# Optimization experiments

Measured on AMD Instinct MI355X. Metric: run time of the kernel, lower is better.

Reference implementation:

```python
import jax, jax.numpy as jnp
import numpy as np

B, S, HID = 4, 2048, 576
NH, NKV, HD = 9, 3, 64
MAXPOS, THETA = 8192, 100000.0


def rotate_half(x):
    x1, x2 = x[..., : x.shape[-1] // 2], x[..., x.shape[-1] // 2 :]
    return jnp.concatenate((-x2, x1), axis=-1)


def setup_inputs() -> dict:
    key = jax.random.key(0)
    ks = jax.random.split(key, 6)
    x = jax.random.normal(ks[0], (B, S, HID), dtype=jnp.float32)
    # RoPE tables (HuggingFace layout: freqs duplicated across halves)
    inv_freq = 1.0 / (THETA ** (np.arange(0, HD, 2, dtype=np.float32) / HD))
    freqs = np.outer(np.arange(MAXPOS, dtype=np.float32), inv_freq)
    emb = np.concatenate([freqs, freqs], axis=-1)
    cos = jnp.asarray(np.cos(emb))
    sin = jnp.asarray(np.sin(emb))
    position_ids = jnp.broadcast_to(jnp.arange(S, dtype=jnp.int64), (B, S))
    # additive causal mask [B,1,S,S]
    causal = jnp.where(
        jnp.tril(jnp.ones((S, S), dtype=bool)), 0.0, -1e9
    ).astype(jnp.float32)
    attention_mask = jnp.broadcast_to(causal, (B, 1, S, S))
    scale = 0.02
    wq = jax.random.normal(ks[1], (NH * HD, HID), dtype=jnp.float32) * scale
    wk = jax.random.normal(ks[2], (NKV * HD, HID), dtype=jnp.float32) * scale
    wv = jax.random.normal(ks[3], (NKV * HD, HID), dtype=jnp.float32) * scale
    wo = jax.random.normal(ks[4], (HID, NH * HD), dtype=jnp.float32) * scale
    return {
        "x": x, "cos": cos, "sin": sin, "position_ids": position_ids,
        "attention_mask": attention_mask,
        "wq": wq, "wk": wk, "wv": wv, "wo": wo,
    }


def reference(x, cos, sin, position_ids, attention_mask, wq, wk, wv, wo):
    b, s, _ = x.shape
    # projections (nn.Linear: y = x @ W.T), split into heads -> [B,H,S,D]
    q = (x @ wq.T).reshape(b, s, NH, HD).transpose(0, 2, 1, 3)
    k = (x @ wk.T).reshape(b, s, NKV, HD).transpose(0, 2, 1, 3)
    v = (x @ wv.T).reshape(b, s, NKV, HD).transpose(0, 2, 1, 3)
    # RoPE: cos/sin gathered per position -> [B,1,S,D], broadcast over heads
    c = cos[position_ids][:, None, :, :]
    si = sin[position_ids][:, None, :, :]
    q = q * c + rotate_half(q) * si
    k = k * c + rotate_half(k) * si
    # GQA expansion: repeat_interleave kv heads to match q heads
    k = jnp.repeat(k, NH // NKV, axis=1)
    v = jnp.repeat(v, NH // NKV, axis=1)
    scale = 1.0 / jnp.sqrt(jnp.asarray(HD, dtype=x.dtype))
    scores = jnp.einsum("bhqd,bhkd->bhqk", q, k) * scale + attention_mask
    attn = jax.nn.softmax(scores.astype(jnp.float32), axis=-1).astype(q.dtype)
    out = jnp.einsum("bhqk,bhkd->bhqd", attn, v)
    out = out.transpose(0, 2, 1, 3).reshape(b, s, NH * HD)
    return out @ wo.T
```

## Files before the change

kernel.cpp:

```cpp
#include <hip/hip_runtime.h>
#include <hip/hip_bf16.h>

#define B_    4
#define S_    2048
#define HID_  576
#define NH_   9
#define NKV_  3
#define HD_   64
#define GQ_   3

typedef __attribute__((ext_vector_type(8))) short bf16x8;
typedef __attribute__((ext_vector_type(4))) float f32x4;
typedef __attribute__((ext_vector_type(16))) float f32x16;

__device__ __forceinline__ short f2bf(float f) {
    union { float f; unsigned int u; } v; v.f = f;
    unsigned int r = (v.u + 0x7fffu + ((v.u >> 16) & 1u)) >> 16;
    return (short)r;
}

__device__ __forceinline__ unsigned int cvt_pk_bf16(float a, float b) {
    unsigned int r;
    asm("v_cvt_pk_bf16_f32 %0, %1, %2" : "=v"(r) : "v"(a), "v"(b));
    return r;
}

__device__ __forceinline__ float exp2fast(float x) {
    return __builtin_amdgcn_exp2f(x);
}

__device__ __forceinline__ void async16(const void* g, void* l) {
    __builtin_amdgcn_global_load_lds(
        (const __attribute__((address_space(1))) unsigned int*)g,
        (__attribute__((address_space(3))) unsigned int*)l, 16, 0, 0);
}

#define NX_   (8192 * 576)
#define NWQ_  (576 * 576)
#define NWK_  (192 * 576)
#define NWV_  (192 * 576)
#define NWO_  (576 * 576)
#define NTOT_ (NX_ + NWQ_ + NWK_ + NWV_ + NWO_)

__global__ __launch_bounds__(256) void convert_kernel(
    const float* __restrict__ x,  const float* __restrict__ wq,
    const float* __restrict__ wk, const float* __restrict__ wv,
    const float* __restrict__ wo,
    short* __restrict__ xb, short* __restrict__ wqkvb, short* __restrict__ wob)
{
    int i4 = (blockIdx.x * 256 + threadIdx.x) * 4;
    const float* src; short* dst;
    if (i4 < NX_)                          { src = x  + i4;                          dst = xb    + i4; }
    else if (i4 < NX_ + NWQ_)              { src = wq + (i4 - NX_);                  dst = wqkvb + (i4 - NX_); }
    else if (i4 < NX_ + NWQ_ + NWK_)       { src = wk + (i4 - NX_ - NWQ_);           dst = wqkvb + (i4 - NX_); }
    else if (i4 < NX_ + NWQ_ + NWK_ + NWV_){ src = wv + (i4 - NX_ - NWQ_ - NWK_);    dst = wqkvb + (i4 - NX_); }
    else                                   { src = wo + (i4 - NX_ - NWQ_ - NWK_ - NWV_);
                                             dst = wob + (i4 - NX_ - NWQ_ - NWK_ - NWV_); }
    float4 v = *(const float4*)src;
    short4 o = make_short4(f2bf(v.x), f2bf(v.y), f2bf(v.z), f2bf(v.w));
    *(short4*)dst = o;
}

__global__ __launch_bounds__(256) void qkv_kernel(
    const short* __restrict__ xb,
    const short* __restrict__ wqkvb,
    const float* __restrict__ cosb,
    const float* __restrict__ sinb,
    short* __restrict__ Q,
    short* __restrict__ K,
    short* __restrict__ Vt)
{
    __shared__ __align__(16) short As[2][256 * 64];
    __shared__ __align__(16) short Bs[2][64 * 64];

    const int bid = blockIdx.x;
    const int f   = (bid & 7) * 60 + (bid >> 3);
    const int m0     = (f / 15) * 256;
    const int nb_blk = f % 15;
    const int tid  = threadIdx.x;
    const int w    = tid >> 6, lane = tid & 63;
    const int quad = lane >> 4, c = lane & 15;
    const int lr   = lane >> 3, lg = lane & 7;
    const int sw   = lg ^ lr;
    const int xg   = quad ^ (c & 7);

    auto stage = [&](int step, short* dstA, short* dstB) {
        const int k0 = step * 64;
        #pragma unroll
        for (int r = 0; r < 8; ++r) {
            int ch = w * 8 + r, R = ch * 8 + lr;
            async16(xb + (size_t)(m0 + R) * HID_ + k0 + sw * 8, (char*)dstA + ch * 1024);
        }
        #pragma unroll
        for (int r = 0; r < 2; ++r) {
            int ch = w * 2 + r, R = ch * 8 + lr;
            async16(wqkvb + (size_t)(nb_blk * 64 + R) * HID_ + k0 + sw * 8, (char*)dstB + ch * 1024);
        }
    };

    f32x4 acc[4][4];
    #pragma unroll
    for (int mt = 0; mt < 4; ++mt)
        #pragma unroll
        for (int nb = 0; nb < 4; ++nb) acc[mt][nb] = (f32x4){0.f, 0.f, 0.f, 0.f};

    stage(0, As[0], Bs[0]);

    int buf = 0;
    for (int kk = 0; kk < 9; ++kk) {
        __syncthreads();
        if (kk < 8) stage(kk + 1, As[buf ^ 1], Bs[buf ^ 1]);

        const short* a_s = As[buf];
        const short* b_s = Bs[buf];
        bf16x8 bfr[4][2];
        #pragma unroll
        for (int nb = 0; nb < 4; ++nb) {
            int row = nb * 16 + c;
            bfr[nb][0] = *(const bf16x8*)(b_s + row * 64 + xg * 8);
            bfr[nb][1] = *(const bf16x8*)(b_s + row * 64 + (xg ^ 4) * 8);
        }
        #pragma unroll
        for (int mt = 0; mt < 4; ++mt) {
            int row = w * 64 + mt * 16 + c;
            bf16x8 a0 = *(const bf16x8*)(a_s + row * 64 + xg * 8);
            bf16x8 a1 = *(const bf16x8*)(a_s + row * 64 + (xg ^ 4) * 8);
            #pragma unroll
            for (int nb = 0; nb < 4; ++nb) {
                acc[mt][nb] = __builtin_amdgcn_mfma_f32_16x16x32_bf16(a0, bfr[nb][0], acc[mt][nb], 0, 0, 0);
                acc[mt][nb] = __builtin_amdgcn_mfma_f32_16x16x32_bf16(a1, bfr[nb][1], acc[mt][nb], 0, 0, 0);
            }
        }
        buf ^= 1;
    }

    int type, head;
    if (nb_blk < NH_)            { type = 0; head = nb_blk; }
    else if (nb_blk < NH_ + NKV_){ type = 1; head = nb_blk - NH_; }
    else                         { type = 2; head = nb_blk - NH_ - NKV_; }
    const int b  = m0 >> 11;
    const int s0 = m0 & (S_ - 1);

    if (type < 2) {
        const float qs = (type == 0) ? 0.18033688f : 1.0f;
        #pragma unroll
        for (int mt = 0; mt < 4; ++mt)
            #pragma unroll
            for (int reg = 0; reg < 4; ++reg) {
                int s = s0 + w * 64 + mt * 16 + quad * 4 + reg;
                const float* cr = cosb + (size_t)s * HD_;
                const float* sr = sinb + (size_t)s * HD_;
                float a0 = acc[mt][0][reg], a1 = acc[mt][1][reg];
                float a2 = acc[mt][2][reg], a3 = acc[mt][3][reg];
                float o0 = (a0 * cr[c]      - a2 * sr[c])      * qs;
                float o1 = (a1 * cr[c + 16] - a3 * sr[c + 16]) * qs;
                float o2 = (a2 * cr[c + 32] + a0 * sr[c + 32]) * qs;
                float o3 = (a3 * cr[c + 48] + a1 * sr[c + 48]) * qs;
                short* dst = (type == 0)
                    ? Q + (((size_t)b * NH_  + head) * S_ + s) * HD_
                    : K + (((size_t)b * NKV_ + head) * S_ + s) * HD_;
                dst[c]      = f2bf(o0);
                dst[c + 16] = f2bf(o1);
                dst[c + 32] = f2bf(o2);
                dst[c + 48] = f2bf(o3);
            }
    } else {
        short* base = Vt + (((size_t)b * NKV_ + head) * HD_) * S_;
        #pragma unroll
        for (int mt = 0; mt < 4; ++mt) {
            int s4 = s0 + w * 64 + mt * 16 + quad * 4;
            #pragma unroll
            for (int nb = 0; nb < 4; ++nb) {
                int d = nb * 16 + c;
                short4 pk = make_short4(f2bf(acc[mt][nb][0]), f2bf(acc[mt][nb][1]),
                                        f2bf(acc[mt][nb][2]), f2bf(acc[mt][nb][3]));
                *(short4*)(base + (size_t)d * S_ + s4) = pk;
            }
        }
    }
}

__global__ __launch_bounds__(256) void attn_kernel(
    const short* __restrict__ Q,
    const short* __restrict__ K,
    const short* __restrict__ Vt,
    short* __restrict__ AOb)
{
    __shared__ __align__(16) char smem[32768];
    short* KsB = (short*)smem;
    short* VsB = (short*)(smem + 16384);

    const int hb = blockIdx.x;
    const int h  = hb >> 2, b = hb & 3;
    const int qt = 31 - blockIdx.y;
    const int kh = h / GQ_;
    const int tid  = threadIdx.x;
    const int w    = tid >> 6, lane = tid & 63;
    const int l31  = lane & 31, hi = lane >> 5, l7 = lane & 7;
    const int lr   = lane >> 3, lg = lane & 7;
    const int sw   = lg ^ lr;
    const int qh   = w >> 1, kv = w & 1;

    const short* Qg = Q  + (((size_t)b * NH_  + h ) * S_ + qt * 64) * HD_;
    const short* Kg = K  + (((size_t)b * NKV_ + kh) * S_) * HD_;
    const short* Vg = Vt + (((size_t)b * NKV_ + kh) * HD_) * S_;

    bf16x8 aq[4];
    #pragma unroll
    for (int ks = 0; ks < 4; ++ks)
        aq[ks] = *(const bf16x8*)(Qg + (size_t)(qh * 32 + l31) * HD_ + (2 * ks + hi) * 8);

    const bool stK = (w < 2);
    const int  ch0 = (w & 1) * 4;
    const short* gs[4];
    #pragma unroll
    for (int r = 0; r < 4; ++r) {
        int ch = ch0 + r;
        gs[r] = stK ? Kg + (size_t)(ch * 8 + lr) * HD_ + sw * 8
                    : Vg + (size_t)(ch * 8 + lr) * S_  + sw * 8;
    }
    const int gstep = stK ? 64 * HD_ : 64;

    #pragma unroll
    for (int r = 0; r < 4; ++r)
        async16(gs[r], (char*)(stK ? KsB : VsB) + (ch0 + r) * 1024);

    f32x16 acc_o[2];
    #pragma unroll
    for (int dt = 0; dt < 2; ++dt)
        #pragma unroll
        for (int i = 0; i < 16; ++i) acc_o[dt][i] = 0.f;
    float acc_ls = 0.f;

    auto do_tile = [&](const short* ksb, const short* vsb, bool MASK) {
        if (MASK && kv > qh) return;
        f32x16 z;
        #pragma unroll
        for (int i = 0; i < 16; ++i) z[i] = 0.f;
        #pragma unroll
        for (int ks = 0; ks < 4; ++ks) {
            bf16x8 ak = *(const bf16x8*)(ksb + (kv * 32 + l31) * 64 + ((2 * ks + hi) ^ l7) * 8);
            z = __builtin_amdgcn_mfma_f32_32x32x16_bf16(ak, aq[ks], z, 0, 0, 0);
        }
        float p[16];
        #pragma unroll
        for (int r = 0; r < 16; ++r) {
            float pv = exp2fast(z[r] - 4.0f);
            if (MASK && kv == qh && ((r & 3) + 8 * (r >> 2) + 4 * hi > l31)) pv = 0.f;
            p[r] = pv;
        }
        float lp = 0.f;
        #pragma unroll
        for (int r = 0; r < 16; ++r) lp += p[r];
        acc_ls += lp;
        #pragma unroll
        for (int k2 = 0; k2 < 2; ++k2) {
            unsigned int u0 = cvt_pk_bf16(p[k2 * 8 + 0], p[k2 * 8 + 1]);
            unsigned int u1 = cvt_pk_bf16(p[k2 * 8 + 2], p[k2 * 8 + 3]);
            unsigned int v0 = cvt_pk_bf16(p[k2 * 8 + 4], p[k2 * 8 + 5]);
            unsigned int v1 = cvt_pk_bf16(p[k2 * 8 + 6], p[k2 * 8 + 7]);
            asm("v_permlane32_swap_b32 %0, %1" : "+v"(u0), "+v"(v0));
            asm("v_permlane32_swap_b32 %0, %1" : "+v"(u1), "+v"(v1));
            union { unsigned int u[4]; bf16x8 v8; } af;
            af.u[0] = u0; af.u[1] = u1; af.u[2] = v0; af.u[3] = v1;
            #pragma unroll
            for (int dt = 0; dt < 2; ++dt) {
                bf16x8 bv = *(const bf16x8*)(vsb + (dt * 32 + l31) * 64 + ((kv * 4 + k2 * 2 + hi) ^ l7) * 8);
                acc_o[dt] = __builtin_amdgcn_mfma_f32_32x32x16_bf16(af.v8, bv, acc_o[dt], 0, 0, 0);
            }
        }
    };

    __syncthreads();
    int buf = 0;
    for (int kt = 0; kt < qt; ++kt) {
        #pragma unroll
        for (int r = 0; r < 4; ++r) {
            gs[r] += gstep;
            async16(gs[r], (char*)(stK ? KsB : VsB) + (buf ^ 1) * 8192 + (ch0 + r) * 1024);
        }
        do_tile(KsB + buf * 4096, VsB + buf * 4096, false);
        __syncthreads();
        buf ^= 1;
    }
    do_tile(KsB + buf * 4096, VsB + buf * 4096, true);

    float ls2 = acc_ls + __shfl_xor(acc_ls, 32);
    float* sc  = (float*)smem;
    float* scl = sc + 4096;
    __syncthreads();
    if (kv == 1) {
        #pragma unroll
        for (int dt = 0; dt < 2; ++dt)
            #pragma unroll
            for (int r = 0; r < 16; ++r)
                sc[qh * 2048 + (dt * 16 + r) * 64 + lane] = acc_o[dt][r];
        if (lane < 32) scl[qh * 32 + lane] = ls2;
    }
    __syncthreads();
    if (kv == 0) {
        #pragma unroll
        for (int dt = 0; dt < 2; ++dt)
            #pragma unroll
            for (int r = 0; r < 16; ++r)
                acc_o[dt][r] += sc[qh * 2048 + (dt * 16 + r) * 64 + lane];
        float lt = ls2 + scl[qh * 32 + l31];
        float linv = 1.0f / lt;
        if (lane < 32) scl[qh * 32 + lane] = linv;
        #pragma unroll
        for (int dt = 0; dt < 2; ++dt)
            #pragma unroll
            for (int r = 0; r < 16; ++r) {
                int q = (r & 3) + 8 * (r >> 2) + 4 * hi;
                int s = qt * 64 + qh * 32 + q;
                float li = scl[qh * 32 + q];
                AOb[(((size_t)b * S_ + s) * NH_ + h) * HD_ + dt * 32 + l31] =
                    f2bf(acc_o[dt][r] * li);
            }
    }
}

__global__ __launch_bounds__(256) void oproj_kernel(
    const short* __restrict__ AOb,
    const short* __restrict__ wob,
    float* __restrict__ out)
{
    __shared__ __align__(16) short As[2][256 * 64];
    __shared__ __align__(16) short Bs[2][64 * 64];

    const int bid = blockIdx.x;
    const int f   = (bid & 7) * 36 + (bid >> 3);
    const int m0 = (f / 9) * 256;
    const int n0 = (f % 9) * 64;
    const int tid  = threadIdx.x;
    const int w    = tid >> 6, lane = tid & 63;
    const int quad = lane >> 4, c = lane & 15;
    const int lr   = lane >> 3, lg = lane & 7;
    const int sw   = lg ^ lr;
    const int xg   = quad ^ (c & 7);

    auto stage = [&](int step, short* dstA, short* dstB) {
        const int k0 = step * 64;
        #pragma unroll
        for (int r = 0; r < 8; ++r) {
            int ch = w * 8 + r, R = ch * 8 + lr;
            async16(AOb + (size_t)(m0 + R) * HID_ + k0 + sw * 8, (char*)dstA + ch * 1024);
        }
        #pragma unroll
        for (int r = 0; r < 2; ++r) {
            int ch = w * 2 + r, R = ch * 8 + lr;
            async16(wob + (size_t)(n0 + R) * HID_ + k0 + sw * 8, (char*)dstB + ch * 1024);
        }
    };

    f32x4 acc[4][4];
    #pragma unroll
    for (int mt = 0; mt < 4; ++mt)
        #pragma unroll
        for (int nb = 0; nb < 4; ++nb) acc[mt][nb] = (f32x4){0.f, 0.f, 0.f, 0.f};

    stage(0, As[0], Bs[0]);

    int buf = 0;
    for (int kk = 0; kk < 9; ++kk) {
        __syncthreads();
        if (kk < 8) stage(kk + 1, As[buf ^ 1], Bs[buf ^ 1]);

        const short* a_s = As[buf];
        const short* b_s = Bs[buf];
        bf16x8 bfr[4][2];
        #pragma unroll
        for (int nb = 0; nb < 4; ++nb) {
            int row = nb * 16 + c;
            bfr[nb][0] = *(const bf16x8*)(b_s + row * 64 + xg * 8);
            bfr[nb][1] = *(const bf16x8*)(b_s + row * 64 + (xg ^ 4) * 8);
        }
        #pragma unroll
        for (int mt = 0; mt < 4; ++mt) {
            int row = w * 64 + mt * 16 + c;
            bf16x8 a0 = *(const bf16x8*)(a_s + row * 64 + xg * 8);
            bf16x8 a1 = *(const bf16x8*)(a_s + row * 64 + (xg ^ 4) * 8);
            #pragma unroll
            for (int nb = 0; nb < 4; ++nb) {
                acc[mt][nb] = __builtin_amdgcn_mfma_f32_16x16x32_bf16(a0, bfr[nb][0], acc[mt][nb], 0, 0, 0);
                acc[mt][nb] = __builtin_amdgcn_mfma_f32_16x16x32_bf16(a1, bfr[nb][1], acc[mt][nb], 0, 0, 0);
            }
        }
        buf ^= 1;
    }

    #pragma unroll
    for (int mt = 0; mt < 4; ++mt)
        #pragma unroll
        for (int reg = 0; reg < 4; ++reg) {
            int m = m0 + w * 64 + mt * 16 + quad * 4 + reg;
            float* dst = out + (size_t)m * HID_ + n0;
            #pragma unroll
            for (int nb = 0; nb < 4; ++nb)
                dst[nb * 16 + c] = acc[mt][nb][reg];
        }
}

extern "C" void kernel_launch(void* const* d_in, const int* in_sizes, int n_in,
                              void* d_out, int out_size, void* d_ws, size_t ws_size,
                              hipStream_t stream) {
    const float* x    = (const float*)d_in[0];
    const float* cosb = (const float*)d_in[1];
    const float* sinb = (const float*)d_in[2];
    const float* wq   = (const float*)d_in[5];
    const float* wk   = (const float*)d_in[6];
    const float* wv   = (const float*)d_in[7];
    const float* wo   = (const float*)d_in[8];

    short* xb    = (short*)d_ws;
    short* wqkvb = xb    + (size_t)NX_;
    short* wob   = wqkvb + (size_t)(NWQ_ + NWK_ + NWV_);
    short* Qb    = wob   + (size_t)NWO_;
    short* Kb    = Qb    + (size_t)B_ * NH_  * S_ * HD_;
    short* Vtb   = Kb    + (size_t)B_ * NKV_ * S_ * HD_;
    short* AOb   = Vtb   + (size_t)B_ * NKV_ * S_ * HD_;

    convert_kernel<<<dim3(NTOT_ / 4 / 256), dim3(256), 0, stream>>>(
        x, wq, wk, wv, wo, xb, wqkvb, wob);
    qkv_kernel<<<dim3(480), dim3(256), 0, stream>>>(
        xb, wqkvb, cosb, sinb, Qb, Kb, Vtb);
    attn_kernel<<<dim3(36, 32), dim3(256), 0, stream>>>(Qb, Kb, Vtb, AOb);
    oproj_kernel<<<dim3(288), dim3(256), 0, stream>>>(AOb, wob, (float*)d_out);
}
```

Measured before the change: 186.3 us.

## Process 128 query rows per attention block to halve K/V tile reloads

The attention kernel now covers 128 query rows per block instead of 64, with each warp holding two 32-row Q groups that share one K/V tile load from shared memory. The grid is halved and causal skipping moves to a per-32-row-group check. It also folds the -4 bias into the accumulator's initial value and raises wave priority around the MFMA sections. The cost is more registers per wave (double accumulators), which may lower occupancy, and fewer blocks to spread across CUs.

```diff
diff --git a/kernel.cpp b/kernel.cpp
--- a/kernel.cpp
+++ b/kernel.cpp
@@ -186,13 +186,13 @@
     const short* __restrict__ Vt,
     short* __restrict__ AOb)
 {
-    __shared__ __align__(16) char smem[32768];
+    __shared__ __align__(16) char smem[33280];
     short* KsB = (short*)smem;
     short* VsB = (short*)(smem + 16384);
 
     const int hb = blockIdx.x;
     const int h  = hb >> 2, b = hb & 3;
-    const int qt = 31 - blockIdx.y;
+    const int qt2 = 15 - blockIdx.y;
     const int kh = h / GQ_;
     const int tid  = threadIdx.x;
     const int w    = tid >> 6, lane = tid & 63;
@@ -200,15 +200,19 @@
     const int lr   = lane >> 3, lg = lane & 7;
     const int sw   = lg ^ lr;
     const int qh   = w >> 1, kv = w & 1;
-
-    const short* Qg = Q  + (((size_t)b * NH_  + h ) * S_ + qt * 64) * HD_;
+    const int qb0  = qt2 * 128 + qh * 64;
+    const int nkt  = 2 * qt2 + 2;
+
+    const short* Qg = Q  + (((size_t)b * NH_  + h ) * S_) * HD_;
     const short* Kg = K  + (((size_t)b * NKV_ + kh) * S_) * HD_;
     const short* Vg = Vt + (((size_t)b * NKV_ + kh) * HD_) * S_;
 
-    bf16x8 aq[4];
-    #pragma unroll
-    for (int ks = 0; ks < 4; ++ks)
-        aq[ks] = *(const bf16x8*)(Qg + (size_t)(qh * 32 + l31) * HD_ + (2 * ks + hi) * 8);
+    bf16x8 aq[2][4];
+    #pragma unroll
+    for (int qg = 0; qg < 2; ++qg)
+        #pragma unroll
+        for (int ks = 0; ks < 4; ++ks)
+            aq[qg][ks] = *(const bf16x8*)(Qg + (size_t)(qb0 + qg * 32 + l31) * HD_ + (2 * ks + hi) * 8);
 
     const bool stK = (w < 2);
     const int  ch0 = (w & 1) * 4;
@@ -225,98 +229,126 @@
     for (int r = 0; r < 4; ++r)
         async16(gs[r], (char*)(stK ? KsB : VsB) + (ch0 + r) * 1024);
 
-    f32x16 acc_o[2];
-    #pragma unroll
-    for (int dt = 0; dt < 2; ++dt)
-        #pragma unroll
-        for (int i = 0; i < 16; ++i) acc_o[dt][i] = 0.f;
-    float acc_ls = 0.f;
-
-    auto do_tile = [&](const short* ksb, const short* vsb, bool MASK) {
-        if (MASK && kv > qh) return;
-        f32x16 z;
-        #pragma unroll
-        for (int i = 0; i < 16; ++i) z[i] = 0.f;
-        #pragma unroll
-        for (int ks = 0; ks < 4; ++ks) {
-            bf16x8 ak = *(const bf16x8*)(ksb + (kv * 32 + l31) * 64 + ((2 * ks + hi) ^ l7) * 8);
-            z = __builtin_amdgcn_mfma_f32_32x32x16_bf16(ak, aq[ks], z, 0, 0, 0);
-        }
-        float p[16];
-        #pragma unroll
-        for (int r = 0; r < 16; ++r) {
-            float pv = exp2fast(z[r] - 4.0f);
-            if (MASK && kv == qh && ((r & 3) + 8 * (r >> 2) + 4 * hi > l31)) pv = 0.f;
-            p[r] = pv;
-        }
-        float lp = 0.f;
-        #pragma unroll
-        for (int r = 0; r < 16; ++r) lp += p[r];
-        acc_ls += lp;
-        #pragma unroll
-        for (int k2 = 0; k2 < 2; ++k2) {
-            unsigned int u0 = cvt_pk_bf16(p[k2 * 8 + 0], p[k2 * 8 + 1]);
-            unsigned int u1 = cvt_pk_bf16(p[k2 * 8 + 2], p[k2 * 8 + 3]);
-            unsigned int v0 = cvt_pk_bf16(p[k2 * 8 + 4], p[k2 * 8 + 5]);
-            unsigned int v1 = cvt_pk_bf16(p[k2 * 8 + 6], p[k2 * 8 + 7]);
-            asm("v_permlane32_swap_b32 %0, %1" : "+v"(u0), "+v"(v0));
-            asm("v_permlane32_swap_b32 %0, %1" : "+v"(u1), "+v"(v1));
-            union { unsigned int u[4]; bf16x8 v8; } af;
-            af.u[0] = u0; af.u[1] = u1; af.u[2] = v0; af.u[3] = v1;
-            #pragma unroll
-            for (int dt = 0; dt < 2; ++dt) {
-                bf16x8 bv = *(const bf16x8*)(vsb + (dt * 32 + l31) * 64 + ((kv * 4 + k2 * 2 + hi) ^ l7) * 8);
-                acc_o[dt] = __builtin_amdgcn_mfma_f32_32x32x16_bf16(af.v8, bv, acc_o[dt], 0, 0, 0);
+    f32x16 acc_o[2][2];
+    #pragma unroll
+    for (int qg = 0; qg < 2; ++qg)
+        #pragma unroll
+        for (int dt = 0; dt < 2; ++dt)
+            #pragma unroll
+            for (int i = 0; i < 16; ++i) acc_o[qg][dt][i] = 0.f;
+    float acc_ls[2] = {0.f, 0.f};
+
+    auto do_tile = [&](const short* ksb, const short* vsb, int kt) {
+        const int kb = kt * 64 + kv * 32;
+        if (qb0 + 32 < kb) return;
+        bf16x8 ak[4];
+        #pragma unroll
+        for (int ks = 0; ks < 4; ++ks)
+            ak[ks] = *(const bf16x8*)(ksb + (kv * 32 + l31) * 64 + ((2 * ks + hi) ^ l7) * 8);
+        #pragma unroll
+        for (int qg = 0; qg < 2; ++qg) {
+            const int qb = qb0 + qg * 32;
+            if (qb < kb) continue;
+            const bool diag = (qb == kb);
+            f32x16 z;
+            #pragma unroll
+            for (int i = 0; i < 16; ++i) z[i] = -4.0f;
+            __builtin_amdgcn_s_setprio(1);
+            #pragma unroll
+            for (int ks = 0; ks < 4; ++ks)
+                z = __builtin_amdgcn_mfma_f32_32x32x16_bf16(ak[ks], aq[qg][ks], z, 0, 0, 0);
+            __builtin_amdgcn_s_setprio(0);
+            float p[16];
+            #pragma unroll
+            for (int r = 0; r < 16; ++r) {
+                float pv = exp2fast(z[r]);
+                if (diag && ((r & 3) + 8 * (r >> 2) + 4 * hi > l31)) pv = 0.f;
+                p[r] = pv;
+            }
+            float lp = 0.f;
+            #pragma unroll
+            for (int r = 0; r < 16; ++r) lp += p[r];
+            acc_ls[qg] += lp;
+            #pragma unroll
+            for (int k2 = 0; k2 < 2; ++k2) {
+                unsigned int u0 = cvt_pk_bf16(p[k2 * 8 + 0], p[k2 * 8 + 1]);
+                unsigned int u1 = cvt_pk_bf16(p[k2 * 8 + 2], p[k2 * 8 + 3]);
+                unsigned int v0 = cvt_pk_bf16(p[k2 * 8 + 4], p[k2 * 8 + 5]);
+                unsigned int v1 = cvt_pk_bf16(p[k2 * 8 + 6], p[k2 * 8 + 7]);
+                asm("v_permlane32_swap_b32 %0, %1" : "+v"(u0), "+v"(v0));
+                asm("v_permlane32_swap_b32 %0, %1" : "+v"(u1), "+v"(v1));
+                union { unsigned int u[4]; bf16x8 v8; } af;
+                af.u[0] = u0; af.u[1] = u1; af.u[2] = v0; af.u[3] = v1;
+                __builtin_amdgcn_s_setprio(1);
+                #pragma unroll
+                for (int dt = 0; dt < 2; ++dt) {
+                    bf16x8 bv = *(const bf16x8*)(vsb + (dt * 32 + l31) * 64 + ((kv * 4 + k2 * 2 + hi) ^ l7) * 8);
+                    acc_o[qg][dt] = __builtin_amdgcn_mfma_f32_32x32x16_bf16(af.v8, bv, acc_o[qg][dt], 0, 0, 0);
+                }
+                __builtin_amdgcn_s_setprio(0);
             }
         }
     };
 
     __syncthreads();
     int buf = 0;
-    for (int kt = 0; kt < qt; ++kt) {
+    for (int kt = 0; kt < nkt - 1; ++kt) {
         #pragma unroll
         for (int r = 0; r < 4; ++r) {
             gs[r] += gstep;
             async16(gs[r], (char*)(stK ? KsB : VsB) + (buf ^ 1) * 8192 + (ch0 + r) * 1024);
         }
-        do_tile(KsB + buf * 4096, VsB + buf * 4096, false);
+        do_tile(KsB + buf * 4096, VsB + buf * 4096, kt);
         __syncthreads();
         buf ^= 1;
     }
-    do_tile(KsB + buf * 4096, VsB + buf * 4096, true);
-
-    float ls2 = acc_ls + __shfl_xor(acc_ls, 32);
+    do_tile(KsB + buf * 4096, VsB + buf * 4096, nkt - 1);
+
+    float ls2[2];
+    #pragma unroll
+    for (int qg = 0; qg < 2; ++qg)
+        ls2[qg] = acc_ls[qg] + __shfl_xor(acc_ls[qg], 32);
     float* sc  = (float*)smem;
-    float* scl = sc + 4096;
+    float* scl = (float*)(smem + 32768);
     __syncthreads();
     if (kv == 1) {
         #pragma unroll
-        for (int dt = 0; dt < 2; ++dt)
-            #pragma unroll
-            for (int r = 0; r < 16; ++r)
-                sc[qh * 2048 + (dt * 16 + r) * 64 + lane] = acc_o[dt][r];
-        if (lane < 32) scl[qh * 32 + lane] = ls2;
+        for (int qg = 0; qg < 2; ++qg)
+            #pragma unroll
+            for (int dt = 0; dt < 2; ++dt)
+                #pragma unroll
+                for (int r = 0; r < 16; ++r)
+                    sc[(((qh * 2 + qg) * 2 + dt) * 16 + r) * 64 + lane] = acc_o[qg][dt][r];
+        if (lane < 32) {
+            scl[(qh * 2 + 0) * 32 + lane] = ls2[0];
+            scl[(qh * 2 + 1) * 32 + lane] = ls2[1];
+        }
     }
     __syncthreads();
     if (kv == 0) {
         #pragma unroll
-        for (int dt = 0; dt < 2; ++dt)
-            #pragma unroll
-            for (int r = 0; r < 16; ++r)
-                acc_o[dt][r] += sc[qh * 2048 + (dt * 16 + r) * 64 + lane];
-        float lt = ls2 + scl[qh * 32 + l31];
-        float linv = 1.0f / lt;
-        if (lane < 32) scl[qh * 32 + lane] = linv;
-        #pragma unroll
-        for (int dt = 0; dt < 2; ++dt)
-            #pragma unroll
-            for (int r = 0; r < 16; ++r) {
-                int q = (r & 3) + 8 * (r >> 2) + 4 * hi;
-                int s = qt * 64 + qh * 32 + q;
-                float li = scl[qh * 32 + q];
-                AOb[(((size_t)b * S_ + s) * NH_ + h) * HD_ + dt * 32 + l31] =
-                    f2bf(acc_o[dt][r] * li);
-            }
+        for (int qg = 0; qg < 2; ++qg) {
+            #pragma unroll
+            for (int dt = 0; dt < 2; ++dt)
+                #pragma unroll
+                for (int r = 0; r < 16; ++r)
+                    acc_o[qg][dt][r] += sc[(((qh * 2 + qg) * 2 + dt) * 16 + r) * 64 + lane];
+            float lt = ls2[qg] + scl[(qh * 2 + qg) * 32 + l31];
+            float linv = 1.0f / lt;
+            if (lane < 32) scl[(qh * 2 + qg) * 32 + lane] = linv;
+        }
+        #pragma unroll
+        for (int qg = 0; qg < 2; ++qg)
+            #pragma unroll
+            for (int dt = 0; dt < 2; ++dt)
+                #pragma unroll
+                for (int r = 0; r < 16; ++r) {
+                    int q = (r & 3) + 8 * (r >> 2) + 4 * hi;
+                    int s = qb0 + qg * 32 + q;
+                    float li = scl[(qh * 2 + qg) * 32 + q];
+                    AOb[(((size_t)b * S_ + s) * NH_ + h) * HD_ + dt * 32 + l31] =
+                        f2bf(acc_o[qg][dt][r] * li);
+                }
     }
 }
 
@@ -424,6 +456,6 @@
         x, wq, wk, wv, wo, xb, wqkvb, wob);
     qkv_kernel<<<dim3(480), dim3(256), 0, stream>>>(
         xb, wqkvb, cosb, sinb, Qb, Kb, Vtb);
-    attn_kernel<<<dim3(36, 32), dim3(256), 0, stream>>>(Qb, Kb, Vtb, AOb);
+    attn_kernel<<<dim3(36, 16), dim3(256), 0, stream>>>(Qb, Kb, Vtb, AOb);
     oproj_kernel<<<dim3(288), dim3(256), 0, stream>>>(AOb, wob, (float*)d_out);
 }
```

Measured after the change: 193.5 us. 1.04x slower.
